# Performance work log

Hardware: AMD Instinct MI355X
Metric: run time of the kernel (lower is better)

Reference implementation:

```python
import jax, jax.numpy as jnp
import numpy as np

B, IMG, P, D, H, HD, DEPTH, MLPD = 32, 224, 16, 768, 12, 64, 12, 3072
N = (IMG // P) ** 2 + 1  # 197 tokens incl. cls
TASKS, PL, NPL = 10, 5, 5
SCALE = HD ** -0.5


def _ln(x, w, b, eps=1e-6):
    m = jnp.mean(x, -1, keepdims=True)
    v = jnp.var(x, -1, keepdims=True)
    return (x - m) * jax.lax.rsqrt(v + eps) * w + b


def setup_inputs():
    key = jax.random.key(0)
    ks = jax.random.split(key, 16)
    g = lambda k, shape: (jax.random.normal(k, shape) * 0.02).astype(jnp.float32)
    return dict(
        x=jax.random.normal(ks[0], (B, 3, IMG, IMG), jnp.float32),
        task_id=jax.random.randint(ks[1], (B,), 0, TASKS),
        patch_w=g(ks[2], (D, 3, P, P)), patch_b=jnp.zeros((D,), jnp.float32),
        cls_token=g(ks[3], (1, 1, D)), pos_embed=g(ks[4], (1, N, D)),
        ln1_w=jnp.ones((DEPTH, D)), ln1_b=jnp.zeros((DEPTH, D)),
        qkv_w=g(ks[5], (DEPTH, 3 * D, D)), qkv_b=jnp.zeros((DEPTH, 3 * D)),
        proj_w=g(ks[6], (DEPTH, D, D)), proj_b=jnp.zeros((DEPTH, D)),
        ln2_w=jnp.ones((DEPTH, D)), ln2_b=jnp.zeros((DEPTH, D)),
        fc1_w=g(ks[7], (DEPTH, MLPD, D)), fc1_b=jnp.zeros((DEPTH, MLPD)),
        fc2_w=g(ks[8], (DEPTH, D, MLPD)), fc2_b=jnp.zeros((DEPTH, D)),
        norm_w=jnp.ones((D,)), norm_b=jnp.zeros((D,)),
        prefix_k=g(ks[9], (NPL, TASKS, PL, H, HD)),
        prefix_v=g(ks[10], (NPL, TASKS, PL, H, HD)),
        act_scale=jnp.ones((NPL, 2, 1, 1), jnp.float32),
    )


def reference(x, task_id, patch_w, patch_b, cls_token, pos_embed, ln1_w, ln1_b,
              qkv_w, qkv_b, proj_w, proj_b, ln2_w, ln2_b, fc1_w, fc1_b,
              fc2_w, fc2_b, norm_w, norm_b, prefix_k, prefix_v, act_scale):
    tid = jnp.clip(task_id, 0, TASKS - 1)
    Bx = x.shape[0]
    # patch embed: conv stride P -> [B, D, 14, 14] -> [B, 196, D]
    h = jax.lax.conv_general_dilated(x, patch_w, (P, P), 'VALID',
                                     dimension_numbers=('NCHW', 'OIHW', 'NCHW'))
    h = h.reshape(Bx, D, -1).transpose(0, 2, 1) + patch_b
    h = jnp.concatenate([jnp.broadcast_to(cls_token, (Bx, 1, D)), h], axis=1)
    h = h + pos_embed
    for i in range(DEPTH):
        xn = _ln(h, ln1_w[i], ln1_b[i])
        qkv = (xn @ qkv_w[i].T + qkv_b[i]).reshape(Bx, N, 3, H, HD)
        q, k, v = [jnp.transpose(qkv[:, :, j], (0, 2, 1, 3)) for j in range(3)]  # [B,H,N,HD]
        if i < NPL:
            kp = jnp.transpose(prefix_k[i][tid], (0, 2, 1, 3))  # [B,H,PL,HD]
            vp = jnp.transpose(prefix_v[i][tid], (0, 2, 1, 3))
            k = jnp.concatenate([kp, k], axis=2)
            v = jnp.concatenate([vp, v], axis=2)
        logits = jnp.einsum('bhqd,bhkd->bhqk', q, k) * SCALE
        if i < NPL:
            s = act_scale[i]  # [2,1,1]
            pp = logits[..., :PL]
            pp = pp + jax.nn.sigmoid(pp * s[0]) * s[1]  # norga gating on prefix logits
            logits = jnp.concatenate([pp, logits[..., PL:]], axis=-1)
        probs = jax.nn.softmax(logits, axis=-1)
        attn = jnp.einsum('bhqk,bhkd->bhqd', probs, v)
        attn = attn.transpose(0, 2, 1, 3).reshape(Bx, N, D)
        h = h + attn @ proj_w[i].T + proj_b[i]
        yn = _ln(h, ln2_w[i], ln2_b[i])
        y = jax.nn.gelu(yn @ fc1_w[i].T + fc1_b[i], approximate=False)
        h = h + y @ fc2_w[i].T + fc2_b[i]
    h = _ln(h, norm_w, norm_b)
    return h[:, 0]
```

## Files before the change

kernel.cpp:

```cpp
#include <hip/hip_runtime.h>
#include <hip/hip_bf16.h>

#define B_     32
#define NTOK   197
#define NPATCH 196
#define D_     768
#define H_     12
#define HD_    64
#define DEPTH_ 12
#define MLPD_  3072
#define TASKS_ 10
#define PL_    5
#define NPL_   5
#define SCALE_ 0.125f
#define ROWS   (B_*NTOK)

typedef unsigned short ushortT;
typedef __bf16 bf16x8 __attribute__((ext_vector_type(8)));
typedef float  f32x4  __attribute__((ext_vector_type(4)));

__device__ inline unsigned int f2bf(float f){
  unsigned int u = __float_as_uint(f);
  return (u + 0x7fffu + ((u >> 16) & 1u)) >> 16;
}
__device__ inline float gelu_f(float x){ return 0.5f * x * (1.f + erff(x * 0.70710678118f)); }

__device__ inline void gload16(const void* g, void* l){
  __builtin_amdgcn_global_load_lds(
      (const __attribute__((address_space(1))) void*)(uintptr_t)g,
      (__attribute__((address_space(3))) void*)(uintptr_t)l,
      16, 0, 0);
}

__global__ __launch_bounds__(256) void convw4_kernel(const float* __restrict__ s0,
    const float* __restrict__ s1, const float* __restrict__ s2, const float* __restrict__ s3,
    ushortT* __restrict__ dst)
{
  int idx = blockIdx.x * 256 + threadIdx.x;
  int e = idx * 8;
  if (e >= 7077888) return;
  const float* s; int loc;
  if (e < 1769472)      { s = s0; loc = e; }
  else if (e < 2359296) { s = s1; loc = e - 1769472; }
  else if (e < 4718592) { s = s2; loc = e - 2359296; }
  else                  { s = s3; loc = e - 4718592; }
  float4 a = *(const float4*)(s + loc);
  float4 c = *(const float4*)(s + loc + 4);
  uint4 o;
  o.x = f2bf(a.x) | (f2bf(a.y) << 16);
  o.y = f2bf(a.z) | (f2bf(a.w) << 16);
  o.z = f2bf(c.x) | (f2bf(c.y) << 16);
  o.w = f2bf(c.z) | (f2bf(c.w) << 16);
  *(uint4*)(dst + e) = o;
}

__global__ __launch_bounds__(256) void convw1_kernel(const float* __restrict__ s,
    ushortT* __restrict__ dst, int n8)
{
  int idx = blockIdx.x * 256 + threadIdx.x;
  if (idx >= n8) return;
  int e = idx * 8;
  float4 a = *(const float4*)(s + e);
  float4 c = *(const float4*)(s + e + 4);
  uint4 o;
  o.x = f2bf(a.x) | (f2bf(a.y) << 16);
  o.y = f2bf(a.z) | (f2bf(a.w) << 16);
  o.z = f2bf(c.x) | (f2bf(c.y) << 16);
  o.w = f2bf(c.z) | (f2bf(c.w) << 16);
  *(uint4*)(dst + e) = o;
}

__global__ __launch_bounds__(256) void im2col_kernel(const float* __restrict__ x,
                                                     ushortT* __restrict__ out)
{
  int idx = blockIdx.x * 256 + threadIdx.x;
  const int tot = B_ * NPATCH * D_;
  if (idx >= tot) return;
  int m = idx / D_, k = idx - m * D_;
  int b = m / NPATCH, p = m - b * NPATCH;
  int pr = p / 14, pc = p - pr * 14;
  int c = k >> 8, r = k & 255;
  int py = r >> 4, px = r & 15;
  float v = x[(((size_t)(b * 3 + c) * 224) + pr * 16 + py) * 224 + pc * 16 + px];
  out[idx] = (ushortT)f2bf(v);
}

__global__ __launch_bounds__(256) void assemble_kernel(const float* __restrict__ pe,
    const float* __restrict__ patch_b, const float* __restrict__ cls,
    const float* __restrict__ pos, float* __restrict__ h)
{
  int idx = blockIdx.x * 256 + threadIdx.x;
  const int tot = ROWS * D_;
  if (idx >= tot) return;
  int bn = idx / D_, d = idx - bn * D_;
  int b = bn / NTOK, n = bn - b * NTOK;
  float v;
  if (n == 0) v = cls[d];
  else        v = pe[((size_t)b * NPATCH + (n - 1)) * D_ + d] + patch_b[d];
  h[idx] = v + pos[(size_t)n * D_ + d];
}

template<int OUTBF>
__global__ __launch_bounds__(256) void ln_kernel(const float* __restrict__ x, size_t xstride,
    const float* __restrict__ w, const float* __restrict__ b,
    void* __restrict__ y, size_t ystride)
{
  const float* xr = x + (size_t)blockIdx.x * xstride;
  float vals[3];
  float s = 0.f, ss = 0.f;
  #pragma unroll
  for (int t = 0; t < 3; t++) {
    float v = xr[threadIdx.x + t * 256];
    vals[t] = v; s += v; ss += v * v;
  }
  #pragma unroll
  for (int off = 32; off >= 1; off >>= 1) {
    s  += __shfl_down(s, off);
    ss += __shfl_down(ss, off);
  }
  __shared__ float sm[4], ssm[4];
  int wid = threadIdx.x >> 6, lane = threadIdx.x & 63;
  if (lane == 0) { sm[wid] = s; ssm[wid] = ss; }
  __syncthreads();
  s  = sm[0] + sm[1] + sm[2] + sm[3];
  ss = ssm[0] + ssm[1] + ssm[2] + ssm[3];
  float mean = s * (1.f / D_);
  float var  = ss * (1.f / D_) - mean * mean;
  float inv  = rsqrtf(var + 1e-6f);
  #pragma unroll
  for (int t = 0; t < 3; t++) {
    int d = threadIdx.x + t * 256;
    float v = (vals[t] - mean) * inv * w[d] + b[d];
    if (OUTBF) ((ushortT*)y)[(size_t)blockIdx.x * ystride + d] = (ushortT)f2bf(v);
    else       ((float*)y)  [(size_t)blockIdx.x * ystride + d] = v;
  }
}

template<int OUTBF, int ACT, int HASRES>
__global__ __launch_bounds__(256) void gemm_mfma(
    const ushortT* __restrict__ A, const ushortT* __restrict__ W,
    const float* __restrict__ bias, const float* __restrict__ resid,
    void* __restrict__ Cout, int M, int N, int K)
{
  __shared__ ushortT As[2][128 * 32];
  __shared__ ushortT Ws[2][128 * 32];
  const int tid = threadIdx.x, lane = tid & 63, wid = tid >> 6;
  const int bm = blockIdx.y * 128, bn = blockIdx.x * 128;
  const int wm = (wid >> 1) * 64, wn = (wid & 1) * 64;

  const int srow = lane >> 2;
  const int scol = (lane & 3) * 8;
  int arow0 = bm + (2 * wid) * 16 + srow;     if (arow0 > M - 1) arow0 = M - 1;
  int arow1 = bm + (2 * wid + 1) * 16 + srow; if (arow1 > M - 1) arow1 = M - 1;
  const int wrow0 = bn + (2 * wid) * 16 + srow;
  const int wrow1 = bn + (2 * wid + 1) * 16 + srow;
  const ushortT* aP0 = A + (size_t)arow0 * K + scol;
  const ushortT* aP1 = A + (size_t)arow1 * K + scol;
  const ushortT* wP0 = W + (size_t)wrow0 * K + scol;
  const ushortT* wP1 = W + (size_t)wrow1 * K + scol;
  const int c0 = (2 * wid) * 512, c1 = (2 * wid + 1) * 512;

  f32x4 acc[4][4];
  #pragma unroll
  for (int i = 0; i < 4; i++)
    #pragma unroll
    for (int j = 0; j < 4; j++)
      acc[i][j] = (f32x4){0.f, 0.f, 0.f, 0.f};

  const int rsel = lane & 15, ksel = (lane >> 4) * 8;
  const int nk = K >> 5;

  gload16(aP0, As[0] + c0); gload16(aP1, As[0] + c1);
  gload16(wP0, Ws[0] + c0); gload16(wP1, Ws[0] + c1);
  __syncthreads();

  for (int kt = 0; kt < nk; ++kt) {
    const int cur = kt & 1;
    if (kt + 1 < nk) {
      const int off = (kt + 1) * 32;
      gload16(aP0 + off, As[cur ^ 1] + c0); gload16(aP1 + off, As[cur ^ 1] + c1);
      gload16(wP0 + off, Ws[cur ^ 1] + c0); gload16(wP1 + off, Ws[cur ^ 1] + c1);
    }
    bf16x8 af[4], bfr[4];
    #pragma unroll
    for (int i = 0; i < 4; i++)
      af[i] = *(const bf16x8*)(As[cur] + (wm + i * 16 + rsel) * 32 + ksel);
    #pragma unroll
    for (int j = 0; j < 4; j++)
      bfr[j] = *(const bf16x8*)(Ws[cur] + (wn + j * 16 + rsel) * 32 + ksel);
    #pragma unroll
    for (int i = 0; i < 4; i++)
      #pragma unroll
      for (int j = 0; j < 4; j++)
        acc[i][j] = __builtin_amdgcn_mfma_f32_16x16x32_bf16(af[i], bfr[j], acc[i][j], 0, 0, 0);
    __syncthreads();
  }

  const int crow = (lane >> 4) * 4, ccol = lane & 15;
  #pragma unroll
  for (int i = 0; i < 4; i++) {
    #pragma unroll
    for (int r = 0; r < 4; r++) {
      int m = bm + wm + i * 16 + crow + r;
      if (m < M) {
        #pragma unroll
        for (int j = 0; j < 4; j++) {
          int n = bn + wn + j * 16 + ccol;
          float v = acc[i][j][r];
          if (bias) v += bias[n];
          if (ACT) v = gelu_f(v);
          if (HASRES) v += resid[(size_t)m * N + n];
          if (OUTBF) ((ushortT*)Cout)[(size_t)m * N + n] = (ushortT)f2bf(v);
          else       ((float*)Cout)  [(size_t)m * N + n] = v;
        }
      }
    }
  }
}

#define KROWS 208
#define VSTR  232
__global__ __launch_bounds__(256) void attn_mfma(
    const ushortT* __restrict__ qkv, const float* __restrict__ prefix_k,
    const float* __restrict__ prefix_v, const float* __restrict__ act_scale,
    const int* __restrict__ task_id, ushortT* __restrict__ out,
    int layer, int koff)
{
  __shared__ ushortT smem[13312 + 14848 + 4096];
  ushortT* Kl = smem;
  ushortT* Vt = smem + 13312;
  ushortT* Ps = smem + 13312 + 14848;

  const int tid = threadIdx.x, lane = tid & 63, wid = tid >> 6;
  const int g = lane >> 4, qc = lane & 15;
  const int qh = blockIdx.x, h = blockIdx.y, b = blockIdx.z;
  const int KtA = NTOK + koff;

  int tsk = 0;
  float s0 = 1.f, s1 = 1.f;
  if (koff) {
    tsk = task_id[b]; tsk = tsk < 0 ? 0 : (tsk > TASKS_ - 1 ? TASKS_ - 1 : tsk);
    s0 = act_scale[layer * 2]; s1 = act_scale[layer * 2 + 1];
  }

  {
    uint4* vz = (uint4*)Vt;
    for (int i = tid; i < 14848 / 8; i += 256) vz[i] = (uint4){0, 0, 0, 0};
    uint4* kz = (uint4*)(Kl + 202 * 64);
    if (tid < 48) kz[tid] = (uint4){0, 0, 0, 0};
  }
  __syncthreads();

  for (int u = tid; u < KtA * 8; u += 256) {
    int row = u >> 3, cg = u & 7;
    uint4 val;
    if (row < koff) {
      size_t off = ((((size_t)layer * TASKS_ + tsk) * PL_ + row) * H_ + h) * HD_ + cg * 8;
      float4 f0 = *(const float4*)(prefix_k + off);
      float4 f1 = *(const float4*)(prefix_k + off + 4);
      val.x = f2bf(f0.x) | (f2bf(f0.y) << 16); val.y = f2bf(f0.z) | (f2bf(f0.w) << 16);
      val.z = f2bf(f1.x) | (f2bf(f1.y) << 16); val.w = f2bf(f1.z) | (f2bf(f1.w) << 16);
    } else {
      int n = row - koff;
      val = *(const uint4*)(qkv + ((size_t)b * NTOK + n) * 2304 + D_ + h * HD_ + cg * 8);
    }
    *(uint4*)(Kl + row * 64 + ((cg * 8) ^ ((row & 7) << 3))) = val;
  }
  for (int u = tid; u < KtA * 8; u += 256) {
    int row = u >> 3, dg = u & 7;
    ushortT e[8];
    if (row < koff) {
      size_t off = ((((size_t)layer * TASKS_ + tsk) * PL_ + row) * H_ + h) * HD_ + dg * 8;
      #pragma unroll
      for (int t = 0; t < 8; t++) e[t] = (ushortT)f2bf(prefix_v[off + t]);
    } else {
      int n = row - koff;
      uint4 v = *(const uint4*)(qkv + ((size_t)b * NTOK + n) * 2304 + 2 * D_ + h * HD_ + dg * 8);
      *(uint4*)e = v;
    }
    #pragma unroll
    for (int t = 0; t < 8; t++) Vt[(dg * 8 + t) * VSTR + row] = e[t];
  }
  __syncthreads();

  const int tend = qh ? 13 : 7;
  for (int t = qh * 7 + wid; t < tend; t += 4) {
    const int q0 = t * 16;
    int qr = q0 + qc; if (qr > NTOK - 1) qr = NTOK - 1;
    const ushortT* qp = qkv + ((size_t)b * NTOK + qr) * 2304 + h * HD_ + g * 8;
    bf16x8 qf0 = *(const bf16x8*)qp;
    bf16x8 qf1 = *(const bf16x8*)(qp + 32);

    f32x4 sacc[13];
    #pragma unroll
    for (int kt = 0; kt < 13; kt++) sacc[kt] = (f32x4){0.f, 0.f, 0.f, 0.f};
    #pragma unroll
    for (int kt = 0; kt < 13; kt++) {
      int row = kt * 16 + qc;
      int sw = (row & 7) << 3;
      bf16x8 ka0 = *(const bf16x8*)(Kl + row * 64 + ((g * 8) ^ sw));
      bf16x8 ka1 = *(const bf16x8*)(Kl + row * 64 + ((32 + g * 8) ^ sw));
      sacc[kt] = __builtin_amdgcn_mfma_f32_16x16x32_bf16(ka0, qf0, sacc[kt], 0, 0, 0);
      sacc[kt] = __builtin_amdgcn_mfma_f32_16x16x32_bf16(ka1, qf1, sacc[kt], 0, 0, 0);
    }

    float* sp = (float*)sacc;
    float mx = -1e30f;
    #pragma unroll
    for (int kt = 0; kt < 13; kt++)
      #pragma unroll
      for (int r = 0; r < 4; r++) {
        int k = kt * 16 + g * 4 + r;
        float s = sp[kt * 4 + r] * SCALE_;
        if (koff && k < PL_) s += s1 / (1.f + __expf(-s * s0));
        if (k >= KtA) s = -1e30f;
        sp[kt * 4 + r] = s;
        mx = fmaxf(mx, s);
      }
    mx = fmaxf(mx, __shfl_xor(mx, 16));
    mx = fmaxf(mx, __shfl_xor(mx, 32));
    float sum = 0.f;
    #pragma unroll
    for (int i = 0; i < 52; i++) { float p = __expf(sp[i] - mx); sp[i] = p; sum += p; }
    sum += __shfl_xor(sum, 16);
    sum += __shfl_xor(sum, 32);
    const float inv = 1.f / sum;

    f32x4 oacc[4];
    #pragma unroll
    for (int d = 0; d < 4; d++) oacc[d] = (f32x4){0.f, 0.f, 0.f, 0.f};
    #pragma unroll
    for (int c = 0; c < 7; c++) {
      ushortT* slab = Ps + wid * 1024 + (c & 1) * 512;
      uint2 w0, w1;
      {
        float p0 = sp[8 * c + 0] * inv, p1 = sp[8 * c + 1] * inv;
        float p2 = sp[8 * c + 2] * inv, p3 = sp[8 * c + 3] * inv;
        w0.x = f2bf(p0) | (f2bf(p1) << 16); w0.y = f2bf(p2) | (f2bf(p3) << 16);
      }
      if (c < 6) {
        float p0 = sp[8 * c + 4] * inv, p1 = sp[8 * c + 5] * inv;
        float p2 = sp[8 * c + 6] * inv, p3 = sp[8 * c + 7] * inv;
        w1.x = f2bf(p0) | (f2bf(p1) << 16); w1.y = f2bf(p2) | (f2bf(p3) << 16);
      } else { w1.x = 0; w1.y = 0; }
      *(uint2*)(slab + qc * 32 + g * 4) = w0;
      *(uint2*)(slab + qc * 32 + 16 + g * 4) = w1;
      bf16x8 pa = *(const bf16x8*)(slab + qc * 32 + g * 8);
      #pragma unroll
      for (int dt = 0; dt < 4; dt++) {
        bf16x8 vb = *(const bf16x8*)(Vt + (dt * 16 + qc) * VSTR + c * 32 + g * 8);
        oacc[dt] = __builtin_amdgcn_mfma_f32_16x16x32_bf16(pa, vb, oacc[dt], 0, 0, 0);
      }
    }

    #pragma unroll
    for (int r = 0; r < 4; r++) {
      int q = q0 + g * 4 + r;
      if (q < NTOK) {
        size_t ro = ((size_t)b * NTOK + q) * D_ + h * HD_;
        #pragma unroll
        for (int dt = 0; dt < 4; dt++)
          out[ro + dt * 16 + qc] = (ushortT)f2bf(oacc[dt][r]);
      }
    }
  }
}

extern "C" void kernel_launch(void* const* d_in, const int* in_sizes, int n_in,
                              void* d_out, int out_size, void* d_ws, size_t ws_size,
                              hipStream_t stream)
{
  (void)in_sizes; (void)n_in; (void)out_size; (void)ws_size;
  const float* x         = (const float*)d_in[0];
  const int*   task_id   = (const int*)  d_in[1];
  const float* patch_w   = (const float*)d_in[2];
  const float* patch_b   = (const float*)d_in[3];
  const float* cls_token = (const float*)d_in[4];
  const float* pos_embed = (const float*)d_in[5];
  const float* ln1_w     = (const float*)d_in[6];
  const float* ln1_b     = (const float*)d_in[7];
  const float* qkv_w     = (const float*)d_in[8];
  const float* qkv_b     = (const float*)d_in[9];
  const float* proj_w    = (const float*)d_in[10];
  const float* proj_b    = (const float*)d_in[11];
  const float* ln2_w     = (const float*)d_in[12];
  const float* ln2_b     = (const float*)d_in[13];
  const float* fc1_w     = (const float*)d_in[14];
  const float* fc1_b     = (const float*)d_in[15];
  const float* fc2_w     = (const float*)d_in[16];
  const float* fc2_b     = (const float*)d_in[17];
  const float* norm_w    = (const float*)d_in[18];
  const float* norm_b    = (const float*)d_in[19];
  const float* prefix_k  = (const float*)d_in[20];
  const float* prefix_v  = (const float*)d_in[21];
  const float* act_scale = (const float*)d_in[22];
  float* out = (float*)d_out;

  char* wsb = (char*)d_ws;
  float*   h      = (float*)  (wsb);
  ushortT* actA   = (ushortT*)(wsb + 19365888);
  ushortT* qkvbuf = (ushortT*)(wsb + 29048832);
  ushortT* mlpbuf = (ushortT*)(wsb + 58097664);
  ushortT* wsc    = (ushortT*)(wsb + 96829440);
  float*   peout  = (float*)qkvbuf;

  ushortT* wqkv  = wsc;
  ushortT* wproj = wsc + 1769472;
  ushortT* wfc1  = wsc + 2359296;
  ushortT* wfc2  = wsc + 4718592;

  convw1_kernel<<<288, 256, 0, stream>>>(patch_w, wsc, 73728);
  im2col_kernel<<<(B_ * NPATCH * D_ + 255) / 256, 256, 0, stream>>>(x, actA);
  gemm_mfma<0,0,0><<<dim3(6, 49), 256, 0, stream>>>(
      actA, wsc, nullptr, nullptr, peout, B_ * NPATCH, D_, D_);
  assemble_kernel<<<(ROWS * D_ + 255) / 256, 256, 0, stream>>>(
      peout, patch_b, cls_token, pos_embed, h);

  for (int i = 0; i < DEPTH_; i++) {
    convw4_kernel<<<3456, 256, 0, stream>>>(
        qkv_w + (size_t)i * 1769472, proj_w + (size_t)i * 589824,
        fc1_w + (size_t)i * 2359296, fc2_w + (size_t)i * 2359296, wsc);
    ln_kernel<1><<<ROWS, 256, 0, stream>>>(h, D_, ln1_w + i * D_, ln1_b + i * D_, actA, D_);
    gemm_mfma<1,0,0><<<dim3(18, 50), 256, 0, stream>>>(
        actA, wqkv, qkv_b + i * 3 * D_, nullptr, qkvbuf, ROWS, 3 * D_, D_);
    attn_mfma<<<dim3(2, H_, B_), 256, 0, stream>>>(
        qkvbuf, prefix_k, prefix_v, act_scale, task_id, actA, i, (i < NPL_) ? PL_ : 0);
    gemm_mfma<0,0,1><<<dim3(6, 50), 256, 0, stream>>>(
        actA, wproj, proj_b + i * D_, h, h, ROWS, D_, D_);
    ln_kernel<1><<<ROWS, 256, 0, stream>>>(h, D_, ln2_w + i * D_, ln2_b + i * D_, actA, D_);
    gemm_mfma<1,1,0><<<dim3(24, 50), 256, 0, stream>>>(
        actA, wfc1, fc1_b + i * MLPD_, nullptr, mlpbuf, ROWS, MLPD_, D_);
    gemm_mfma<0,0,1><<<dim3(6, 50), 256, 0, stream>>>(
        mlpbuf, wfc2, fc2_b + i * D_, h, h, ROWS, D_, MLPD_);
  }

  ln_kernel<0><<<B_, 256, 0, stream>>>(h, (size_t)NTOK * D_, norm_w, norm_b, out, D_);
}
```

Baseline: 3.792 ms.

## Triple-buffer GEMM LDS tiles with vmcnt-based waits instead of full syncs

The MFMA GEMM moves from a double-buffered LDS pipeline to a three-stage ring, prefetching three K-tiles ahead. Per-iteration waits now use explicit s_waitcnt vmcnt(8) plus raw s_barrier instead of __syncthreads, so more global loads stay in flight while the MFMAs run. Launch bounds request 3 blocks per CU to keep occupancy with the larger LDS footprint. The tail issues dummy loads at offset 0 to keep the vmcnt counting uniform, which costs some redundant traffic, and correctness relies on gload16 being a direct-to-LDS load tracked by vmcnt.

```diff
diff --git a/kernel.cpp b/kernel.cpp
--- a/kernel.cpp
+++ b/kernel.cpp
@@ -137,13 +137,13 @@
 }
 
 template<int OUTBF, int ACT, int HASRES>
-__global__ __launch_bounds__(256) void gemm_mfma(
+__global__ __launch_bounds__(256, 3) void gemm_mfma(
     const ushortT* __restrict__ A, const ushortT* __restrict__ W,
     const float* __restrict__ bias, const float* __restrict__ resid,
     void* __restrict__ Cout, int M, int N, int K)
 {
-  __shared__ ushortT As[2][128 * 32];
-  __shared__ ushortT Ws[2][128 * 32];
+  __shared__ ushortT As[3][4096];
+  __shared__ ushortT Ws[3][4096];
   const int tid = threadIdx.x, lane = tid & 63, wid = tid >> 6;
   const int bm = blockIdx.y * 128, bn = blockIdx.x * 128;
   const int wm = (wid >> 1) * 64, wn = (wid & 1) * 64;
@@ -170,30 +170,40 @@
   const int rsel = lane & 15, ksel = (lane >> 4) * 8;
   const int nk = K >> 5;
 
-  gload16(aP0, As[0] + c0); gload16(aP1, As[0] + c1);
-  gload16(wP0, Ws[0] + c0); gload16(wP1, Ws[0] + c1);
-  __syncthreads();
-
+  #pragma unroll
+  for (int p = 0; p < 3; ++p) {
+    const int off = p * 32;
+    gload16(aP0 + off, As[p] + c0); gload16(aP1 + off, As[p] + c1);
+    gload16(wP0 + off, Ws[p] + c0); gload16(wP1 + off, Ws[p] + c1);
+  }
+
+  int cb = 0;
   for (int kt = 0; kt < nk; ++kt) {
-    const int cur = kt & 1;
-    if (kt + 1 < nk) {
-      const int off = (kt + 1) * 32;
-      gload16(aP0 + off, As[cur ^ 1] + c0); gload16(aP1 + off, As[cur ^ 1] + c1);
-      gload16(wP0 + off, Ws[cur ^ 1] + c0); gload16(wP1 + off, Ws[cur ^ 1] + c1);
-    }
+    asm volatile("s_waitcnt vmcnt(8)" ::: "memory");
+    __builtin_amdgcn_sched_barrier(0);
+    __builtin_amdgcn_s_barrier();
+
     bf16x8 af[4], bfr[4];
     #pragma unroll
     for (int i = 0; i < 4; i++)
-      af[i] = *(const bf16x8*)(As[cur] + (wm + i * 16 + rsel) * 32 + ksel);
+      af[i] = *(const bf16x8*)(As[cb] + (wm + i * 16 + rsel) * 32 + ksel);
     #pragma unroll
     for (int j = 0; j < 4; j++)
-      bfr[j] = *(const bf16x8*)(Ws[cur] + (wn + j * 16 + rsel) * 32 + ksel);
+      bfr[j] = *(const bf16x8*)(Ws[cb] + (wn + j * 16 + rsel) * 32 + ksel);
     #pragma unroll
     for (int i = 0; i < 4; i++)
       #pragma unroll
       for (int j = 0; j < 4; j++)
         acc[i][j] = __builtin_amdgcn_mfma_f32_16x16x32_bf16(af[i], bfr[j], acc[i][j], 0, 0, 0);
-    __syncthreads();
+
+    __builtin_amdgcn_s_barrier();
+
+    const int nt = kt + 3;
+    const int off = (nt < nk) ? nt * 32 : 0;
+    gload16(aP0 + off, As[cb] + c0); gload16(aP1 + off, As[cb] + c1);
+    gload16(wP0 + off, Ws[cb] + c0); gload16(wP1 + off, Ws[cb] + c1);
+
+    cb = (cb == 2) ? 0 : cb + 1;
   }
 
   const int crow = (lane >> 4) * 4, ccol = lane & 15;
```

New measurement: 3.755 ms. About the same (-1.0%).
